# Optimization experiments

Measured on AMD Instinct MI355X. Metric: run time of the kernel, lower is better.

Reference implementation:

```python
import jax, jax.numpy as jnp
import numpy as np
from jax import lax

WIN = 7
PAD = WIN // 2
K1, K2 = 0.01, 0.03
NP = WIN * WIN
COV_NORM = NP / (NP - 1)  # use_sample_covariance=True


def _dwconv(x, w, channel):
    # depthwise 2D conv, SAME-style explicit padding (torch conv2d padding=pad)
    return lax.conv_general_dilated(
        x, w, window_strides=(1, 1),
        padding=[(PAD, PAD), (PAD, PAD)],
        feature_group_count=channel,
        dimension_numbers=('NCHW', 'OIHW', 'NCHW'))


def setup_inputs() -> dict:
    key = jax.random.key(0)
    k1, k2 = jax.random.split(key)
    B, C, H, W = 64, 1, 384, 384
    gt = jax.random.uniform(k1, (B, C, H, W), dtype=jnp.float32)
    pred = jax.random.uniform(k2, (B, C, H, W), dtype=jnp.float32)
    # uniform (box) window: create_window(7, channel=1, gaussian_weights=False)
    window = jnp.ones((C, 1, WIN, WIN), dtype=jnp.float32) / NP
    return {"gt": gt, "pred": pred, "window": window}


def reference(gt, pred, window):
    channel = gt.shape[1]
    data_range = jnp.max(gt)  # data_range=None default

    ux = _dwconv(gt, window, channel)
    uy = _dwconv(pred, window, channel)
    uxx = _dwconv(gt * gt, window, channel) - ux * ux
    uyy = _dwconv(pred * pred, window, channel) - uy * uy
    uxy = _dwconv(gt * pred, window, channel) - ux * uy

    vx = COV_NORM * uxx
    vy = COV_NORM * uyy
    vxy = COV_NORM * uxy

    C1 = (K1 * data_range) ** 2
    C2 = (K2 * data_range) ** 2

    S = (2.0 * ux * uy + C1) * (2.0 * vxy + C2) / ((ux * ux + uy * uy + C1) * (vx + vy + C2))
    ssim_map = S[:, :, PAD:-PAD, PAD:-PAD]
    return jnp.mean(ssim_map)  # size_average=True, full=False
```

## Files before the change

### kernel.cpp

```cpp
#include <hip/hip_runtime.h>


#define PADW 3
#define BW 128
#define BAND 36
#define NIN (BAND + 6)
#define NCHUNK (NIN / 7)

constexpr int B_ = 64, H_ = 384, W_ = 384;
constexpr int OUTD = W_ - 2 * PADW;
constexpr int NBANDS = (OUTD + BAND - 1) / BAND;
constexpr double NPIX = (double)B_ * OUTD * OUTD;

__device__ __forceinline__ unsigned enc_f(float f) {
    unsigned u = __float_as_uint(f);
    return (u & 0x80000000u) ? ~u : (u | 0x80000000u);
}
__device__ __forceinline__ float dec_f(unsigned e) {
    return __uint_as_float((e & 0x80000000u) ? (e & 0x7fffffffu) : ~e);
}

__global__ void __launch_bounds__(256)
max_kernel(const float4* __restrict__ g4, unsigned* ws_max, int n4) {
    int tid = blockIdx.x * blockDim.x + threadIdx.x;
    int stride = gridDim.x * blockDim.x;
    float m = -3.402823466e38f;
    for (int i = tid; i < n4; i += stride) {
        float4 v = g4[i];
        m = fmaxf(m, fmaxf(fmaxf(v.x, v.y), fmaxf(v.z, v.w)));
    }
#pragma unroll
    for (int off = 32; off > 0; off >>= 1)
        m = fmaxf(m, __shfl_down(m, off));
    __shared__ float sm[4];
    if ((threadIdx.x & 63) == 0) sm[threadIdx.x >> 6] = m;
    __syncthreads();
    if (threadIdx.x == 0) {
        float mm = fmaxf(fmaxf(sm[0], sm[1]), fmaxf(sm[2], sm[3]));
        atomicMax(ws_max, enc_f(mm));
    }
}

__global__ void __launch_bounds__(BW)
ssim_kernel(const float* __restrict__ gt, const float* __restrict__ pred,
            const unsigned* __restrict__ ws_max, double* ws_sum) {
    const int t    = threadIdx.x;
    const int tile = blockIdx.x;
    const int band = blockIdx.y;
    const int b    = blockIdx.z;

    const float dr     = dec_f(*ws_max);
    const float C1     = (0.01f * dr) * (0.01f * dr);
    const float C2     = (0.03f * dr) * (0.03f * dr);
    const float inv49  = 1.0f / 49.0f;
    const float covn   = 49.0f / 48.0f;

    const int w0    = PADW + tile * BW;
    const int cb    = w0 - PADW;
    const int extra = min(BW + 6, W_ - cb) - BW;
    const int row0  = band * BAND;
    const int wcol  = w0 + t;
    const bool active = (wcol <= W_ - 1 - PADW);

    __shared__ float sg[7][BW + 6];
    __shared__ float sp[7][BW + 6];
    __shared__ double sred[2];

    float rx[7], ry[7], rxx[7], ryy[7], rxy[7];
#pragma unroll
    for (int j = 0; j < 7; ++j) { rx[j]=0.f; ry[j]=0.f; rxx[j]=0.f; ryy[j]=0.f; rxy[j]=0.f; }

    float vx = 0.f, vy = 0.f, vxx = 0.f, vyy = 0.f, vxy = 0.f;
    double acc = 0.0;

    const float* gbase = gt   + (size_t)b * H_ * W_;
    const float* pbase = pred + (size_t)b * H_ * W_;

    for (int c = 0; c < NCHUNK; ++c) {
        const int base_ir = row0 + c * 7;
        __syncthreads();
#pragma unroll
        for (int j = 0; j < 7; ++j) {
            const int ir = min(base_ir + j, H_ - 1);
            const float* gr = gbase + (size_t)ir * W_ + cb;
            const float* pr = pbase + (size_t)ir * W_ + cb;
            sg[j][t] = gr[t];
            sp[j][t] = pr[t];
            if (t < 6) {
                sg[j][BW + t] = (t < extra) ? gr[BW + t] : 0.0f;
                sp[j][BW + t] = (t < extra) ? pr[BW + t] : 0.0f;
            }
        }
        __syncthreads();

#pragma unroll
        for (int j = 0; j < 7; ++j) {
            float hx = 0.f, hy = 0.f, hxx = 0.f, hyy = 0.f, hxy = 0.f;
#pragma unroll
            for (int k = 0; k < 7; ++k) {
                float g = sg[j][t + k], p = sp[j][t + k];
                hx += g; hy += p;
                hxx = fmaf(g, g, hxx);
                hyy = fmaf(p, p, hyy);
                hxy = fmaf(g, p, hxy);
            }
            vx  += hx  - rx[j];   rx[j]  = hx;
            vy  += hy  - ry[j];   ry[j]  = hy;
            vxx += hxx - rxx[j];  rxx[j] = hxx;
            vyy += hyy - ryy[j];  ryy[j] = hyy;
            vxy += hxy - rxy[j];  rxy[j] = hxy;

            const int i = c * 7 + j;
            if (i >= 6) {
                const int orow = row0 + i - 6;
                if (active && orow < OUTD) {
                    float ux  = vx * inv49, uy = vy * inv49;
                    float uxx = vxx * inv49 - ux * ux;
                    float uyy = vyy * inv49 - uy * uy;
                    float uxy = vxy * inv49 - ux * uy;
                    float vvx = covn * uxx, vvy = covn * uyy, vvxy = covn * uxy;
                    float num = (2.0f * ux * uy + C1) * (2.0f * vvxy + C2);
                    float den = (ux * ux + uy * uy + C1) * (vvx + vvy + C2);
                    acc += (double)(num / den);
                }
            }
        }
    }

#pragma unroll
    for (int off = 32; off > 0; off >>= 1)
        acc += __shfl_down(acc, off);
    if ((t & 63) == 0) sred[t >> 6] = acc;
    __syncthreads();
    if (t == 0) atomicAdd(ws_sum, sred[0] + sred[1]);
}

__global__ void final_kernel(const double* __restrict__ ws_sum, float* __restrict__ out) {
    out[0] = (float)(ws_sum[0] / NPIX);
}

extern "C" void kernel_launch(void* const* d_in, const int* in_sizes, int n_in,
                              void* d_out, int out_size, void* d_ws, size_t ws_size,
                              hipStream_t stream) {
    const float* gt   = (const float*)d_in[0];
    const float* pred = (const float*)d_in[1];
    float* out = (float*)d_out;

    unsigned* ws_max = (unsigned*)d_ws;
    double*   ws_sum = (double*)((char*)d_ws + 8);

    hipMemsetAsync(d_ws, 0, 16, stream);

    const int n4 = B_ * H_ * W_ / 4;
    max_kernel<<<1024, 256, 0, stream>>>((const float4*)gt, ws_max, n4);

    dim3 grid(3, NBANDS, 64);
    ssim_kernel<<<grid, BW, 0, stream>>>(gt, pred, ws_max, ws_sum);

    final_kernel<<<1, 1, 0, stream>>>(ws_sum, out);
}
```

Before: 160.8 us.

## Process two columns per thread with full-row blocks and fuse final reduction

Each thread now computes two adjacent output columns using float2 loads, sharing the horizontal 7-tap partial sums between them. A block covers a full image row (192 threads) and a 15-row band instead of 128-column tiles and 36-row bands. The separate final kernel is replaced by a last-block-done counter that writes the mean. Smaller bands raise the row-halo reload overhead (21 rows loaded per 15 output rows) in exchange for more blocks and fewer redundant horizontal sums. The shared-memory halo entries sg[j][192..195] are never written but are read by the rightmost threads; this appears harmless because those threads are masked out by the t < 189 check.

```diff
diff --git a/kernel.cpp b/kernel.cpp
--- a/kernel.cpp
+++ b/kernel.cpp
@@ -2,14 +2,16 @@
 
 
 #define PADW 3
-#define BW 128
-#define BAND 36
-#define NIN (BAND + 6)
-#define NCHUNK (NIN / 7)
+#define BT 192
+#define BAND 15
+#define NIN 21
+#define NCHUNK 3
 
 constexpr int B_ = 64, H_ = 384, W_ = 384;
+constexpr int W2 = W_ / 2;
 constexpr int OUTD = W_ - 2 * PADW;
 constexpr int NBANDS = (OUTD + BAND - 1) / BAND;
+constexpr int TOTAL_BLOCKS = NBANDS * B_;
 constexpr double NPIX = (double)B_ * OUTD * OUTD;
 
 __device__ __forceinline__ unsigned enc_f(float f) {
@@ -19,6 +21,9 @@
 __device__ __forceinline__ float dec_f(unsigned e) {
     return __uint_as_float((e & 0x80000000u) ? (e & 0x7fffffffu) : ~e);
 }
+
+__device__ __forceinline__ float2 f2add(float2 a, float2 b) { return make_float2(a.x + b.x, a.y + b.y); }
+__device__ __forceinline__ float2 f2sub(float2 a, float2 b) { return make_float2(a.x - b.x, a.y - b.y); }
 
 __global__ void __launch_bounds__(256)
 max_kernel(const float4* __restrict__ g4, unsigned* ws_max, int n4) {
@@ -41,87 +46,93 @@
     }
 }
 
-__global__ void __launch_bounds__(BW)
+__device__ __forceinline__ float ssim_px(float sx, float sy, float sxx, float syy, float sxy,
+                                         float C1, float C2) {
+    const float inv49 = 1.0f / 49.0f;
+    const float covn  = 49.0f / 48.0f;
+    float ux  = sx * inv49, uy = sy * inv49;
+    float uxx = sxx * inv49 - ux * ux;
+    float uyy = syy * inv49 - uy * uy;
+    float uxy = sxy * inv49 - ux * uy;
+    float vvx = covn * uxx, vvy = covn * uyy, vvxy = covn * uxy;
+    float num = (2.0f * ux * uy + C1) * (2.0f * vvxy + C2);
+    float den = (ux * ux + uy * uy + C1) * (vvx + vvy + C2);
+    return num / den;
+}
+
+__global__ void __launch_bounds__(BT)
 ssim_kernel(const float* __restrict__ gt, const float* __restrict__ pred,
-            const unsigned* __restrict__ ws_max, double* ws_sum) {
+            const unsigned* __restrict__ ws_max, double* ws_sum, unsigned* ws_cnt,
+            float* __restrict__ out) {
     const int t    = threadIdx.x;
-    const int tile = blockIdx.x;
-    const int band = blockIdx.y;
-    const int b    = blockIdx.z;
+    const int band = blockIdx.x;
+    const int b    = blockIdx.y;
 
-    const float dr     = dec_f(*ws_max);
-    const float C1     = (0.01f * dr) * (0.01f * dr);
-    const float C2     = (0.03f * dr) * (0.03f * dr);
-    const float inv49  = 1.0f / 49.0f;
-    const float covn   = 49.0f / 48.0f;
+    const float dr = dec_f(*ws_max);
+    const float C1 = (0.01f * dr) * (0.01f * dr);
+    const float C2 = (0.03f * dr) * (0.03f * dr);
 
-    const int w0    = PADW + tile * BW;
-    const int cb    = w0 - PADW;
-    const int extra = min(BW + 6, W_ - cb) - BW;
-    const int row0  = band * BAND;
-    const int wcol  = w0 + t;
-    const bool active = (wcol <= W_ - 1 - PADW);
+    const int  row0   = band * BAND;
+    const bool active = (t < 189);
 
-    __shared__ float sg[7][BW + 6];
-    __shared__ float sp[7][BW + 6];
-    __shared__ double sred[2];
+    __shared__ float2 sg[7][BT + 4];
+    __shared__ float2 sp[7][BT + 4];
+    __shared__ double sred[3];
 
-    float rx[7], ry[7], rxx[7], ryy[7], rxy[7];
+    float2 rx[7], ry[7], rxx[7], ryy[7], rxy[7];
 #pragma unroll
-    for (int j = 0; j < 7; ++j) { rx[j]=0.f; ry[j]=0.f; rxx[j]=0.f; ryy[j]=0.f; rxy[j]=0.f; }
-
-    float vx = 0.f, vy = 0.f, vxx = 0.f, vyy = 0.f, vxy = 0.f;
+    for (int j = 0; j < 7; ++j) {
+        rx[j] = make_float2(0.f, 0.f); ry[j] = rx[j];
+        rxx[j] = rx[j]; ryy[j] = rx[j]; rxy[j] = rx[j];
+    }
+    float2 vx = make_float2(0.f, 0.f), vy = vx, vxx = vx, vyy = vx, vxy = vx;
     double acc = 0.0;
 
-    const float* gbase = gt   + (size_t)b * H_ * W_;
-    const float* pbase = pred + (size_t)b * H_ * W_;
+    const float2* gbase = (const float2*)(gt   + (size_t)b * H_ * W_);
+    const float2* pbase = (const float2*)(pred + (size_t)b * H_ * W_);
 
     for (int c = 0; c < NCHUNK; ++c) {
-        const int base_ir = row0 + c * 7;
         __syncthreads();
 #pragma unroll
         for (int j = 0; j < 7; ++j) {
-            const int ir = min(base_ir + j, H_ - 1);
-            const float* gr = gbase + (size_t)ir * W_ + cb;
-            const float* pr = pbase + (size_t)ir * W_ + cb;
-            sg[j][t] = gr[t];
-            sp[j][t] = pr[t];
-            if (t < 6) {
-                sg[j][BW + t] = (t < extra) ? gr[BW + t] : 0.0f;
-                sp[j][BW + t] = (t < extra) ? pr[BW + t] : 0.0f;
-            }
+            const int ir = min(row0 + c * 7 + j, H_ - 1);
+            sg[j][t] = gbase[(size_t)ir * W2 + t];
+            sp[j][t] = pbase[(size_t)ir * W2 + t];
         }
         __syncthreads();
 
 #pragma unroll
         for (int j = 0; j < 7; ++j) {
-            float hx = 0.f, hy = 0.f, hxx = 0.f, hyy = 0.f, hxy = 0.f;
-#pragma unroll
-            for (int k = 0; k < 7; ++k) {
-                float g = sg[j][t + k], p = sp[j][t + k];
-                hx += g; hy += p;
-                hxx = fmaf(g, g, hxx);
-                hyy = fmaf(p, p, hyy);
-                hxy = fmaf(g, p, hxy);
-            }
-            vx  += hx  - rx[j];   rx[j]  = hx;
-            vy  += hy  - ry[j];   ry[j]  = hy;
-            vxx += hxx - rxx[j];  rxx[j] = hxx;
-            vyy += hyy - ryy[j];  ryy[j] = hyy;
-            vxy += hxy - rxy[j];  rxy[j] = hxy;
+            float2 d0 = sg[j][t], d1 = sg[j][t + 1], d2 = sg[j][t + 2], d3 = sg[j][t + 3];
+            float2 e0 = sp[j][t], e1 = sp[j][t + 1], e2 = sp[j][t + 2], e3 = sp[j][t + 3];
+
+            float hx0 = d0.x + d0.y + d1.x + d1.y + d2.x + d2.y + d3.x;
+            float hy0 = e0.x + e0.y + e1.x + e1.y + e2.x + e2.y + e3.x;
+            float hxx0 = fmaf(d0.x, d0.x, fmaf(d0.y, d0.y, fmaf(d1.x, d1.x,
+                         fmaf(d1.y, d1.y, fmaf(d2.x, d2.x, fmaf(d2.y, d2.y, d3.x * d3.x))))));
+            float hyy0 = fmaf(e0.x, e0.x, fmaf(e0.y, e0.y, fmaf(e1.x, e1.x,
+                         fmaf(e1.y, e1.y, fmaf(e2.x, e2.x, fmaf(e2.y, e2.y, e3.x * e3.x))))));
+            float hxy0 = fmaf(d0.x, e0.x, fmaf(d0.y, e0.y, fmaf(d1.x, e1.x,
+                         fmaf(d1.y, e1.y, fmaf(d2.x, e2.x, fmaf(d2.y, e2.y, d3.x * e3.x))))));
+
+            float2 h_x  = make_float2(hx0,  hx0  - d0.x        + d3.y);
+            float2 h_y  = make_float2(hy0,  hy0  - e0.x        + e3.y);
+            float2 h_xx = make_float2(hxx0, hxx0 - d0.x * d0.x + d3.y * d3.y);
+            float2 h_yy = make_float2(hyy0, hyy0 - e0.x * e0.x + e3.y * e3.y);
+            float2 h_xy = make_float2(hxy0, hxy0 - d0.x * e0.x + d3.y * e3.y);
+
+            vx  = f2add(vx,  f2sub(h_x,  rx[j]));  rx[j]  = h_x;
+            vy  = f2add(vy,  f2sub(h_y,  ry[j]));  ry[j]  = h_y;
+            vxx = f2add(vxx, f2sub(h_xx, rxx[j])); rxx[j] = h_xx;
+            vyy = f2add(vyy, f2sub(h_yy, ryy[j])); ryy[j] = h_yy;
+            vxy = f2add(vxy, f2sub(h_xy, rxy[j])); rxy[j] = h_xy;
 
             const int i = c * 7 + j;
             if (i >= 6) {
                 const int orow = row0 + i - 6;
                 if (active && orow < OUTD) {
-                    float ux  = vx * inv49, uy = vy * inv49;
-                    float uxx = vxx * inv49 - ux * ux;
-                    float uyy = vyy * inv49 - uy * uy;
-                    float uxy = vxy * inv49 - ux * uy;
-                    float vvx = covn * uxx, vvy = covn * uyy, vvxy = covn * uxy;
-                    float num = (2.0f * ux * uy + C1) * (2.0f * vvxy + C2);
-                    float den = (ux * ux + uy * uy + C1) * (vvx + vvy + C2);
-                    acc += (double)(num / den);
+                    acc += (double)ssim_px(vx.x, vy.x, vxx.x, vyy.x, vxy.x, C1, C2);
+                    acc += (double)ssim_px(vx.y, vy.y, vxx.y, vyy.y, vxy.y, C1, C2);
                 }
             }
         }
@@ -132,11 +143,15 @@
         acc += __shfl_down(acc, off);
     if ((t & 63) == 0) sred[t >> 6] = acc;
     __syncthreads();
-    if (t == 0) atomicAdd(ws_sum, sred[0] + sred[1]);
-}
-
-__global__ void final_kernel(const double* __restrict__ ws_sum, float* __restrict__ out) {
-    out[0] = (float)(ws_sum[0] / NPIX);
+    if (t == 0) {
+        atomicAdd(ws_sum, sred[0] + sred[1] + sred[2]);
+        __threadfence();
+        unsigned prev = atomicAdd(ws_cnt, 1u);
+        if (prev == (unsigned)(TOTAL_BLOCKS - 1)) {
+            double tot = atomicAdd(ws_sum, 0.0);
+            out[0] = (float)(tot / NPIX);
+        }
+    }
 }
 
 extern "C" void kernel_launch(void* const* d_in, const int* in_sizes, int n_in,
@@ -147,6 +162,7 @@
     float* out = (float*)d_out;
 
     unsigned* ws_max = (unsigned*)d_ws;
+    unsigned* ws_cnt = (unsigned*)((char*)d_ws + 4);
     double*   ws_sum = (double*)((char*)d_ws + 8);
 
     hipMemsetAsync(d_ws, 0, 16, stream);
@@ -154,8 +170,6 @@
     const int n4 = B_ * H_ * W_ / 4;
     max_kernel<<<1024, 256, 0, stream>>>((const float4*)gt, ws_max, n4);
 
-    dim3 grid(3, NBANDS, 64);
-    ssim_kernel<<<grid, BW, 0, stream>>>(gt, pred, ws_max, ws_sum);
-
-    final_kernel<<<1, 1, 0, stream>>>(ws_sum, out);
+    dim3 grid(NBANDS, B_);
+    ssim_kernel<<<grid, BT, 0, stream>>>(gt, pred, ws_max, ws_sum, ws_cnt, out);
 }
```

Result: slower. 174.4 us (+8.4%).

## Drop memset and final kernel, use per-block max and last-block finalize

Applied to the files above, without the earlier changes.

Removes the hipMemsetAsync and the single-thread final kernel. The max kernel now writes per-block maxima, which every SSIM block re-reduces, and it also zeroes the accumulators. The last SSIM block, found with an atomic counter, writes the mean. The change also shrinks the row band from 36 to 22 with 4 chunks, giving more blocks with more halo overhead, and swaps the divide for a hardware reciprocal, which slightly reduces precision.

```diff
diff --git a/kernel.cpp b/kernel.cpp
--- a/kernel.cpp
+++ b/kernel.cpp
@@ -3,29 +3,25 @@
 
 #define PADW 3
 #define BW 128
-#define BAND 36
-#define NIN (BAND + 6)
-#define NCHUNK (NIN / 7)
+#define BAND 22
+#define NCHUNK 4
+#define NIN 28
 
 constexpr int B_ = 64, H_ = 384, W_ = 384;
 constexpr int OUTD = W_ - 2 * PADW;
 constexpr int NBANDS = (OUTD + BAND - 1) / BAND;
+constexpr int NTILES = 3;
+constexpr int TOTAL_BLOCKS = NTILES * NBANDS * B_;
+constexpr int NMAXBLK = 256;
 constexpr double NPIX = (double)B_ * OUTD * OUTD;
 
-__device__ __forceinline__ unsigned enc_f(float f) {
-    unsigned u = __float_as_uint(f);
-    return (u & 0x80000000u) ? ~u : (u | 0x80000000u);
-}
-__device__ __forceinline__ float dec_f(unsigned e) {
-    return __uint_as_float((e & 0x80000000u) ? (e & 0x7fffffffu) : ~e);
-}
-
 __global__ void __launch_bounds__(256)
-max_kernel(const float4* __restrict__ g4, unsigned* ws_max, int n4) {
-    int tid = blockIdx.x * blockDim.x + threadIdx.x;
-    int stride = gridDim.x * blockDim.x;
+max_kernel(const float4* __restrict__ g4, float* __restrict__ bmax,
+           double* ws_sum, unsigned* ws_cnt, int n4) {
+    const int t = threadIdx.x;
+    int tid = blockIdx.x * 256 + t;
     float m = -3.402823466e38f;
-    for (int i = tid; i < n4; i += stride) {
+    for (int i = tid; i < n4; i += 256 * NMAXBLK) {
         float4 v = g4[i];
         m = fmaxf(m, fmaxf(fmaxf(v.x, v.y), fmaxf(v.z, v.w)));
     }
@@ -33,27 +29,51 @@
     for (int off = 32; off > 0; off >>= 1)
         m = fmaxf(m, __shfl_down(m, off));
     __shared__ float sm[4];
-    if ((threadIdx.x & 63) == 0) sm[threadIdx.x >> 6] = m;
+    if ((t & 63) == 0) sm[t >> 6] = m;
     __syncthreads();
-    if (threadIdx.x == 0) {
-        float mm = fmaxf(fmaxf(sm[0], sm[1]), fmaxf(sm[2], sm[3]));
-        atomicMax(ws_max, enc_f(mm));
+    if (t == 0) {
+        bmax[blockIdx.x] = fmaxf(fmaxf(sm[0], sm[1]), fmaxf(sm[2], sm[3]));
+        if (blockIdx.x == 0) { *ws_sum = 0.0; *ws_cnt = 0u; }
     }
+}
+
+__device__ __forceinline__ float ssim_px(float sx, float sy, float sxx, float syy, float sxy,
+                                         float C1, float C2) {
+    const float inv49 = 1.0f / 49.0f;
+    const float covn  = 49.0f / 48.0f;
+    float ux  = sx * inv49, uy = sy * inv49;
+    float uxx = sxx * inv49 - ux * ux;
+    float uyy = syy * inv49 - uy * uy;
+    float uxy = sxy * inv49 - ux * uy;
+    float vvx = covn * uxx, vvy = covn * uyy, vvxy = covn * uxy;
+    float num = (2.0f * ux * uy + C1) * (2.0f * vvxy + C2);
+    float den = (ux * ux + uy * uy + C1) * (vvx + vvy + C2);
+    return num * __builtin_amdgcn_rcpf(den);
 }
 
 __global__ void __launch_bounds__(BW)
 ssim_kernel(const float* __restrict__ gt, const float* __restrict__ pred,
-            const unsigned* __restrict__ ws_max, double* ws_sum) {
+            const float* __restrict__ bmax, double* ws_sum, unsigned* ws_cnt,
+            float* __restrict__ out) {
     const int t    = threadIdx.x;
     const int tile = blockIdx.x;
     const int band = blockIdx.y;
     const int b    = blockIdx.z;
 
-    const float dr     = dec_f(*ws_max);
-    const float C1     = (0.01f * dr) * (0.01f * dr);
-    const float C2     = (0.03f * dr) * (0.03f * dr);
-    const float inv49  = 1.0f / 49.0f;
-    const float covn   = 49.0f / 48.0f;
+    __shared__ float sg[7][BW + 6];
+    __shared__ float sp[7][BW + 6];
+    __shared__ float smax[2];
+    __shared__ double sred[2];
+
+    float m = fmaxf(bmax[t], bmax[t + BW]);
+#pragma unroll
+    for (int off = 32; off > 0; off >>= 1)
+        m = fmaxf(m, __shfl_down(m, off));
+    if ((t & 63) == 0) smax[t >> 6] = m;
+    __syncthreads();
+    const float dr = fmaxf(smax[0], smax[1]);
+    const float C1 = (0.01f * dr) * (0.01f * dr);
+    const float C2 = (0.03f * dr) * (0.03f * dr);
 
     const int w0    = PADW + tile * BW;
     const int cb    = w0 - PADW;
@@ -61,10 +81,6 @@
     const int row0  = band * BAND;
     const int wcol  = w0 + t;
     const bool active = (wcol <= W_ - 1 - PADW);
-
-    __shared__ float sg[7][BW + 6];
-    __shared__ float sp[7][BW + 6];
-    __shared__ double sred[2];
 
     float rx[7], ry[7], rxx[7], ryy[7], rxy[7];
 #pragma unroll
@@ -114,14 +130,7 @@
             if (i >= 6) {
                 const int orow = row0 + i - 6;
                 if (active && orow < OUTD) {
-                    float ux  = vx * inv49, uy = vy * inv49;
-                    float uxx = vxx * inv49 - ux * ux;
-                    float uyy = vyy * inv49 - uy * uy;
-                    float uxy = vxy * inv49 - ux * uy;
-                    float vvx = covn * uxx, vvy = covn * uyy, vvxy = covn * uxy;
-                    float num = (2.0f * ux * uy + C1) * (2.0f * vvxy + C2);
-                    float den = (ux * ux + uy * uy + C1) * (vvx + vvy + C2);
-                    acc += (double)(num / den);
+                    acc += (double)ssim_px(vx, vy, vxx, vyy, vxy, C1, C2);
                 }
             }
         }
@@ -132,11 +141,15 @@
         acc += __shfl_down(acc, off);
     if ((t & 63) == 0) sred[t >> 6] = acc;
     __syncthreads();
-    if (t == 0) atomicAdd(ws_sum, sred[0] + sred[1]);
-}
-
-__global__ void final_kernel(const double* __restrict__ ws_sum, float* __restrict__ out) {
-    out[0] = (float)(ws_sum[0] / NPIX);
+    if (t == 0) {
+        atomicAdd(ws_sum, sred[0] + sred[1]);
+        __threadfence();
+        unsigned prev = atomicAdd(ws_cnt, 1u);
+        if (prev == (unsigned)(TOTAL_BLOCKS - 1)) {
+            double tot = atomicAdd(ws_sum, 0.0);
+            out[0] = (float)(tot / NPIX);
+        }
+    }
 }
 
 extern "C" void kernel_launch(void* const* d_in, const int* in_sizes, int n_in,
@@ -146,16 +159,13 @@
     const float* pred = (const float*)d_in[1];
     float* out = (float*)d_out;
 
-    unsigned* ws_max = (unsigned*)d_ws;
-    double*   ws_sum = (double*)((char*)d_ws + 8);
-
-    hipMemsetAsync(d_ws, 0, 16, stream);
+    double*   ws_sum  = (double*)d_ws;
+    unsigned* ws_cnt  = (unsigned*)((char*)d_ws + 8);
+    float*    ws_bmax = (float*)((char*)d_ws + 16);
 
     const int n4 = B_ * H_ * W_ / 4;
-    max_kernel<<<1024, 256, 0, stream>>>((const float4*)gt, ws_max, n4);
+    max_kernel<<<NMAXBLK, 256, 0, stream>>>((const float4*)gt, ws_bmax, ws_sum, ws_cnt, n4);
 
-    dim3 grid(3, NBANDS, 64);
-    ssim_kernel<<<grid, BW, 0, stream>>>(gt, pred, ws_max, ws_sum);
-
-    final_kernel<<<1, 1, 0, stream>>>(ws_sum, out);
+    dim3 grid(NTILES, NBANDS, B_);
+    ssim_kernel<<<grid, BW, 0, stream>>>(gt, pred, ws_bmax, ws_sum, ws_cnt, out);
 }
```

Measured after the change: 302.3 us. 88.0% more time.

## Double-buffer shared row chunks with register prefetch to overlap loads and compute

Applied to the files above, without the earlier changes.

Each 7-row chunk for the next iteration is now loaded into registers before the current chunk is computed, then written into an alternate shared-memory buffer, so only one barrier is needed per chunk. The aim is to hide global-load latency behind the box-filter and SSIM arithmetic. In exchange it raises register pressure (28 extra floats per thread) and doubles shared memory use, which could lower occupancy.

```diff
diff --git a/kernel.cpp b/kernel.cpp
--- a/kernel.cpp
+++ b/kernel.cpp
@@ -62,8 +62,8 @@
     const int wcol  = w0 + t;
     const bool active = (wcol <= W_ - 1 - PADW);
 
-    __shared__ float sg[7][BW + 6];
-    __shared__ float sp[7][BW + 6];
+    __shared__ float sg[2][7][BW + 6];
+    __shared__ float sp[2][7][BW + 6];
     __shared__ double sred[2];
 
     float rx[7], ry[7], rxx[7], ryy[7], rxy[7];
@@ -76,29 +76,49 @@
     const float* gbase = gt   + (size_t)b * H_ * W_;
     const float* pbase = pred + (size_t)b * H_ * W_;
 
-    for (int c = 0; c < NCHUNK; ++c) {
+    float pgv[7], ppv[7], tgv[7], tpv[7];
+
+    auto prefetch = [&](int c) {
         const int base_ir = row0 + c * 7;
-        __syncthreads();
 #pragma unroll
         for (int j = 0; j < 7; ++j) {
             const int ir = min(base_ir + j, H_ - 1);
             const float* gr = gbase + (size_t)ir * W_ + cb;
             const float* pr = pbase + (size_t)ir * W_ + cb;
-            sg[j][t] = gr[t];
-            sp[j][t] = pr[t];
+            pgv[j] = gr[t];
+            ppv[j] = pr[t];
             if (t < 6) {
-                sg[j][BW + t] = (t < extra) ? gr[BW + t] : 0.0f;
-                sp[j][BW + t] = (t < extra) ? pr[BW + t] : 0.0f;
+                tgv[j] = (t < extra) ? gr[BW + t] : 0.0f;
+                tpv[j] = (t < extra) ? pr[BW + t] : 0.0f;
             }
         }
-        __syncthreads();
+    };
+    auto commit = [&](int buf) {
+#pragma unroll
+        for (int j = 0; j < 7; ++j) {
+            sg[buf][j][t] = pgv[j];
+            sp[buf][j][t] = ppv[j];
+            if (t < 6) {
+                sg[buf][j][BW + t] = tgv[j];
+                sp[buf][j][BW + t] = tpv[j];
+            }
+        }
+    };
+
+    prefetch(0);
+    commit(0);
+    __syncthreads();
+
+    for (int c = 0; c < NCHUNK; ++c) {
+        if (c + 1 < NCHUNK) prefetch(c + 1);
+        const int buf = c & 1;
 
 #pragma unroll
         for (int j = 0; j < 7; ++j) {
             float hx = 0.f, hy = 0.f, hxx = 0.f, hyy = 0.f, hxy = 0.f;
 #pragma unroll
             for (int k = 0; k < 7; ++k) {
-                float g = sg[j][t + k], p = sp[j][t + k];
+                float g = sg[buf][j][t + k], p = sp[buf][j][t + k];
                 hx += g; hy += p;
                 hxx = fmaf(g, g, hxx);
                 hyy = fmaf(p, p, hyy);
@@ -124,6 +144,11 @@
                     acc += (double)(num / den);
                 }
             }
+        }
+
+        if (c + 1 < NCHUNK) {
+            commit((c + 1) & 1);
+            __syncthreads();
         }
     }
 
```

Result: slower. 184.5 us (+14.7%).
